# Optimization experiments

Hardware: AMD Instinct MI355X
Metric: run time of the kernel (lower is better)

Reference implementation:

```python
import jax, jax.numpy as jnp
import numpy as np

B, N, D_IMG = 64, 196, 2048
T = 32
V, E, H, A = 32000, 512, 1024, 256
PAD_ID = 0


def setup_inputs() -> dict:
    key = jax.random.key(0)
    ks = jax.random.split(key, 16)
    s = lambda *sh: 1.0 / np.sqrt(sh[-1])
    img_seq = jax.random.normal(ks[0], (B, N, D_IMG), dtype=jnp.float32)
    tokens_in = jax.random.randint(ks[1], (B, T), 0, V, dtype=jnp.int64)
    embed = jax.random.normal(ks[2], (V, E), dtype=jnp.float32) * 0.02
    embed = embed.at[PAD_ID].set(0.0)  # padding_idx row is zero
    W_head1 = jax.random.normal(ks[3], (E, E + D_IMG), dtype=jnp.float32) * s(E + D_IMG)
    W_ih = jax.random.normal(ks[4], (4 * H, E), dtype=jnp.float32) * s(H)
    W_hh = jax.random.normal(ks[5], (4 * H, H), dtype=jnp.float32) * s(H)
    b_ih = jax.random.normal(ks[6], (4 * H,), dtype=jnp.float32) * s(H)
    b_hh = jax.random.normal(ks[7], (4 * H,), dtype=jnp.float32) * s(H)
    W_head = jax.random.normal(ks[8], (V, H), dtype=jnp.float32) * s(H)
    W_img = jax.random.normal(ks[9], (A, D_IMG), dtype=jnp.float32) * s(D_IMG)
    W_hid = jax.random.normal(ks[10], (A, H), dtype=jnp.float32) * s(H)
    w_score = jax.random.normal(ks[11], (A,), dtype=jnp.float32) * s(A)
    W_h0 = jax.random.normal(ks[12], (H, D_IMG), dtype=jnp.float32) * s(D_IMG)
    b_h0 = jax.random.normal(ks[13], (H,), dtype=jnp.float32) * s(D_IMG)
    W_c0 = jax.random.normal(ks[14], (H, D_IMG), dtype=jnp.float32) * s(D_IMG)
    b_c0 = jax.random.normal(ks[15], (H,), dtype=jnp.float32) * s(D_IMG)
    return dict(img_seq=img_seq, tokens_in=tokens_in, embed=embed, W_head1=W_head1,
                W_ih=W_ih, W_hh=W_hh, b_ih=b_ih, b_hh=b_hh, W_head=W_head,
                W_img=W_img, W_hid=W_hid, w_score=w_score,
                W_h0=W_h0, b_h0=b_h0, W_c0=W_c0, b_c0=b_c0)


def _decode(img_seq, tokens_in, embed, W_head1, W_ih, W_hh, b_ih, b_hh,
            W_head, W_img, W_hid, w_score, W_h0, b_h0, W_c0, b_c0):
    g = img_seq.mean(axis=1)                              # [B, D]
    h = jnp.tanh(g @ W_h0.T + b_h0)                       # [B, H]
    c = jnp.tanh(g @ W_c0.T + b_c0)                       # [B, H]
    # image projection is time-invariant: hoist out of the loop
    proj_img = jnp.einsum('bnd,ad->bna', img_seq, W_img)  # [B, N, A]
    emb_all = embed[tokens_in]                            # [B, T, E]

    def step(carry, emb_t):
        h, c = carry
        # additive attention
        proj_h = h @ W_hid.T                              # [B, A]
        scores = jnp.einsum('bna,a->bn', jnp.tanh(proj_img + proj_h[:, None, :]), w_score)
        weights = jax.nn.softmax(scores, axis=-1)         # [B, N]
        ctx = jnp.einsum('bn,bnd->bd', weights, img_seq)  # [B, D]
        x = jnp.concatenate([emb_t, ctx], axis=-1) @ W_head1.T  # [B, E]
        # LSTMCell (PyTorch gate order: i, f, g, o)
        gates = x @ W_ih.T + b_ih + h @ W_hh.T + b_hh     # [B, 4H]
        i, f, gg, o = jnp.split(gates, 4, axis=-1)
        c_new = jax.nn.sigmoid(f) * c + jax.nn.sigmoid(i) * jnp.tanh(gg)
        h_new = jax.nn.sigmoid(o) * jnp.tanh(c_new)
        logits = h_new @ W_head.T                         # [B, V]
        return (h_new, c_new), logits

    _, ys = jax.lax.scan(step, (h, c), jnp.swapaxes(emb_all, 0, 1))  # ys: [T, B, V]
    return jnp.swapaxes(ys, 0, 1)                         # [B, T, V]


def reference(img_seq, tokens_in, embed, W_head1, W_ih, W_hh, b_ih, b_hh,
              W_head, W_img, W_hid, w_score, W_h0, b_h0, W_c0, b_c0):
    return _decode(img_seq, tokens_in, embed, W_head1, W_ih, W_hh, b_ih, b_hh,
                   W_head, W_img, W_hid, w_score, W_h0, b_h0, W_c0, b_c0)
```

## Files before the change

### kernel.cpp

```cpp
#include <hip/hip_runtime.h>
#include <stdint.h>

typedef unsigned short u16;
typedef __bf16 bf16x8 __attribute__((ext_vector_type(8)));
typedef float f32x4 __attribute__((ext_vector_type(4)));

#define DEV static __device__ __forceinline__

DEV u16 f2bu(float f) {
    union { float f; unsigned u; } v; v.f = f;
    unsigned r = v.u + 0x7FFFu + ((v.u >> 16) & 1u);
    return (u16)(r >> 16);
}
DEV float b2f(u16 b) {
    union { unsigned u; float f; } v; v.u = ((unsigned)b) << 16;
    return v.f;
}
DEV float fast_tanh(float x) {
    float e = __expf(2.f * x);
    return 1.f - __fdividef(2.f, e + 1.f);
}
DEV float fast_sig(float x) {
    return __fdividef(1.f, 1.f + __expf(-x));
}
DEV void gload_lds(const u16* g, u16* l) {
    __builtin_amdgcn_global_load_lds((const __attribute__((address_space(1))) void*)g,
                                     (__attribute__((address_space(3))) void*)l, 16, 0, 0);
}

template<bool A_F32, bool B_F32, bool B_KXN, bool OUT_BF16, bool BIAS>
__global__ __launch_bounds__(256) void gemm128(
    const void* __restrict__ Ap, int lda,
    const void* __restrict__ Bp, int ldb,
    void* __restrict__ Cp, int ldc,
    const float* __restrict__ bias, int K)
{
    __shared__ u16 As[128 * 40];
    __shared__ u16 Bs[128 * 40];
    const int tid = threadIdx.x;
    const int lane = tid & 63, wave = tid >> 6;
    const int wr = wave >> 1, wc = wave & 1;
    const int m0 = blockIdx.y * 128, n0 = blockIdx.x * 128;

    f32x4 acc[4][4];
#pragma unroll
    for (int m = 0; m < 4; ++m)
#pragma unroll
        for (int n = 0; n < 4; ++n)
            acc[m][n] = (f32x4){0.f, 0.f, 0.f, 0.f};

    for (int k0 = 0; k0 < K; k0 += 32) {
        __syncthreads();
        if (A_F32) {
            const float* A = (const float*)Ap;
#pragma unroll
            for (int i = 0; i < 4; ++i) {
                int c = tid + i * 256;
                int row = c >> 3, kc = (c & 7) * 4;
                float4 v = *(const float4*)&A[(size_t)(m0 + row) * lda + k0 + kc];
                ushort4 o; o.x = f2bu(v.x); o.y = f2bu(v.y); o.z = f2bu(v.z); o.w = f2bu(v.w);
                *(ushort4*)&As[row * 40 + kc] = o;
            }
        } else {
            const u16* A = (const u16*)Ap;
#pragma unroll
            for (int i = 0; i < 2; ++i) {
                int c = tid + i * 256;
                int row = c >> 2, kc = (c & 3) * 8;
                *(int4*)&As[row * 40 + kc] = *(const int4*)&A[(size_t)(m0 + row) * lda + k0 + kc];
            }
        }
        if (B_KXN) {
            const float* B = (const float*)Bp;
#pragma unroll
            for (int i = 0; i < 4; ++i) {
                int c = tid + i * 256;
                int kk = c >> 5, nc = (c & 31) * 4;
                float4 v = *(const float4*)&B[(size_t)(k0 + kk) * ldb + n0 + nc];
                Bs[(nc + 0) * 40 + kk] = f2bu(v.x);
                Bs[(nc + 1) * 40 + kk] = f2bu(v.y);
                Bs[(nc + 2) * 40 + kk] = f2bu(v.z);
                Bs[(nc + 3) * 40 + kk] = f2bu(v.w);
            }
        } else if (B_F32) {
            const float* B = (const float*)Bp;
#pragma unroll
            for (int i = 0; i < 4; ++i) {
                int c = tid + i * 256;
                int row = c >> 3, kc = (c & 7) * 4;
                float4 v = *(const float4*)&B[(size_t)(n0 + row) * ldb + k0 + kc];
                ushort4 o; o.x = f2bu(v.x); o.y = f2bu(v.y); o.z = f2bu(v.z); o.w = f2bu(v.w);
                *(ushort4*)&Bs[row * 40 + kc] = o;
            }
        } else {
            const u16* B = (const u16*)Bp;
#pragma unroll
            for (int i = 0; i < 2; ++i) {
                int c = tid + i * 256;
                int row = c >> 2, kc = (c & 3) * 8;
                *(int4*)&Bs[row * 40 + kc] = *(const int4*)&B[(size_t)(n0 + row) * ldb + k0 + kc];
            }
        }
        __syncthreads();
        const int fr = lane & 15, kq = (lane >> 4) * 8;
        bf16x8 af[4], bq[4];
#pragma unroll
        for (int m = 0; m < 4; ++m)
            af[m] = *(const bf16x8*)&As[(wr * 64 + m * 16 + fr) * 40 + kq];
#pragma unroll
        for (int n = 0; n < 4; ++n)
            bq[n] = *(const bf16x8*)&Bs[(wc * 64 + n * 16 + fr) * 40 + kq];
#pragma unroll
        for (int m = 0; m < 4; ++m)
#pragma unroll
            for (int n = 0; n < 4; ++n)
                acc[m][n] = __builtin_amdgcn_mfma_f32_16x16x32_bf16(af[m], bq[n], acc[m][n], 0, 0, 0);
    }
    const int fr = lane & 15, rq = (lane >> 4) * 4;
#pragma unroll
    for (int m = 0; m < 4; ++m) {
#pragma unroll
        for (int n = 0; n < 4; ++n) {
            int col = n0 + wc * 64 + n * 16 + fr;
            float bv = BIAS ? bias[col] : 0.f;
#pragma unroll
            for (int r = 0; r < 4; ++r) {
                int row = m0 + wr * 64 + m * 16 + rq + r;
                float v = acc[m][n][r] + bv;
                if (OUT_BF16) ((u16*)Cp)[(size_t)row * ldc + col] = f2bu(v);
                else          ((float*)Cp)[(size_t)row * ldc + col] = v;
            }
        }
    }
}

__global__ __launch_bounds__(512, 4) void gemm_head(const u16* __restrict__ A,
                                                    const u16* __restrict__ B,
                                                    float* __restrict__ C)
{
    __shared__ u16 As[128 * 64];
    __shared__ u16 Bs[256 * 64];
    const int tid = threadIdx.x, lane = tid & 63, wave = tid >> 6;
    const int wr = wave >> 2, wc = wave & 3;
    int bid = blockIdx.x;
    int nb = (bid & 7) * 250 + (bid >> 3);
    const int m0 = (nb & 15) * 128;
    const int n0 = (nb >> 4) * 256;

    f32x4 acc[4][4];
#pragma unroll
    for (int m = 0; m < 4; ++m)
#pragma unroll
        for (int n = 0; n < 4; ++n)
            acc[m][n] = (f32x4){0.f, 0.f, 0.f, 0.f};

    const int srg = lane >> 3;
    const int sslot = lane & 7;
    const int ge = (sslot ^ srg) * 8;
    const int fr = lane & 15, kg = lane >> 4;

    for (int k0 = 0; k0 < 1024; k0 += 64) {
        __syncthreads();
#pragma unroll
        for (int j = 0; j < 2; ++j) {
            const int g = wave * 2 + j;
            gload_lds(&A[(size_t)(m0 + g * 8 + srg) * 1024 + k0 + ge], &As[g * 8 * 64]);
        }
#pragma unroll
        for (int j = 0; j < 4; ++j) {
            const int g = wave * 4 + j;
            gload_lds(&B[(size_t)(n0 + g * 8 + srg) * 1024 + k0 + ge], &Bs[g * 8 * 64]);
        }
        __syncthreads();
#pragma unroll
        for (int kk = 0; kk < 2; ++kk) {
            const int sl = kk * 4 + kg;
            bf16x8 af[4], bq[4];
#pragma unroll
            for (int m = 0; m < 4; ++m) {
                const int row = wr * 64 + m * 16 + fr;
                af[m] = *(const bf16x8*)&As[row * 64 + ((sl ^ (row & 7)) << 3)];
            }
#pragma unroll
            for (int n = 0; n < 4; ++n) {
                const int row = wc * 64 + n * 16 + fr;
                bq[n] = *(const bf16x8*)&Bs[row * 64 + ((sl ^ (row & 7)) << 3)];
            }
#pragma unroll
            for (int m = 0; m < 4; ++m)
#pragma unroll
                for (int n = 0; n < 4; ++n)
                    acc[m][n] = __builtin_amdgcn_mfma_f32_16x16x32_bf16(af[m], bq[n], acc[m][n], 0, 0, 0);
        }
    }
    const int rq = kg * 4;
#pragma unroll
    for (int m = 0; m < 4; ++m)
#pragma unroll
        for (int n = 0; n < 4; ++n) {
            int col = n0 + wc * 64 + n * 16 + fr;
#pragma unroll
            for (int r = 0; r < 4; ++r)
                C[(size_t)(m0 + wr * 64 + m * 16 + rq + r) * 32000 + col] = acc[m][n][r];
        }
}

__global__ __launch_bounds__(256) void prep_k(
    const float* __restrict__ img, const float* __restrict__ Whh,
    const float* __restrict__ Whid, const float* __restrict__ Whead,
    const int* __restrict__ tok, const float* __restrict__ embed,
    const float* __restrict__ bih, const float* __restrict__ bhh,
    u16* __restrict__ img_bf, u16* __restrict__ Whh_bf,
    u16* __restrict__ WhidT, u16* __restrict__ Whead_bf,
    u16* __restrict__ emb_bf, float* __restrict__ bsum)
{
    const int bid = blockIdx.x;
    if (bid < 25088) {
        int i = bid * 256 + threadIdx.x;
        float4 v = ((const float4*)img)[i];
        ushort4 o; o.x = f2bu(v.x); o.y = f2bu(v.y); o.z = f2bu(v.z); o.w = f2bu(v.w);
        ((ushort4*)img_bf)[i] = o;
    } else if (bid < 29184) {
        int i = (bid - 25088) * 256 + threadIdx.x;
        float4 v = ((const float4*)Whh)[i];
        ushort4 o; o.x = f2bu(v.x); o.y = f2bu(v.y); o.z = f2bu(v.z); o.w = f2bu(v.w);
        ((ushort4*)Whh_bf)[i] = o;
    } else if (bid < 29440) {
        int i = (bid - 29184) * 256 + threadIdx.x;
        int a = i >> 8, k4 = (i & 255) * 4;
        float4 v = *(const float4*)&Whid[(size_t)a * 1024 + k4];
        ushort4 o; o.x = f2bu(v.x); o.y = f2bu(v.y); o.z = f2bu(v.z); o.w = f2bu(v.w);
        *(ushort4*)&WhidT[(size_t)(k4 >> 3) * 2048 + a * 8 + (k4 & 7)] = o;
    } else if (bid < 61440) {
        int i = (bid - 29440) * 256 + threadIdx.x;
        float4 v = ((const float4*)Whead)[i];
        ushort4 o; o.x = f2bu(v.x); o.y = f2bu(v.y); o.z = f2bu(v.z); o.w = f2bu(v.w);
        ((ushort4*)Whead_bf)[i] = o;
    } else if (bid < 65536) {
        int id = (bid - 61440) * 256 + threadIdx.x;
        int row = id >> 9, e = id & 511;
        int t = row >> 6, b = row & 63;
        int tk = tok[b * 32 + t];
        emb_bf[(size_t)row * 512 + e] = f2bu(embed[(size_t)tk * 512 + e]);
    } else {
        int i = (bid - 65536) * 256 + threadIdx.x;
        bsum[i] = bih[i] + bhh[i];
    }
}

__global__ __launch_bounds__(256) void pack_w(const u16* __restrict__ Wic,
                                              const u16* __restrict__ Whh,
                                              u16* __restrict__ Wpk)
{
    const int bid = blockIdx.y;
    const int t2 = blockIdx.x * 256 + threadIdx.x;
    const int i = t2 >> 6, lane = t2 & 63;
    const int fr = lane & 15, kq = (lane >> 4) * 8;
    const int grow = ((fr >> 2) << 10) + bid * 4 + (fr & 3);
    const int k0 = i * 32;
    int4 v;
    if (k0 < 2048) v = *(const int4*)&Wic[(size_t)grow * 2048 + k0 + kq];
    else           v = *(const int4*)&Whh[(size_t)grow * 1024 + (k0 - 2048) + kq];
    *(int4*)&Wpk[((size_t)bid * 6144 + t2) * 8] = v;
}

__global__ __launch_bounds__(256) void mean_k(const u16* __restrict__ img_bf, float* __restrict__ gT)
{
    int id = blockIdx.x * 256 + threadIdx.x;
    int b = id >> 10;
    int d = (id & 1023) * 2;
    const u16* base = img_bf + (size_t)b * 196 * 2048 + d;
    float s0 = 0.f, s1 = 0.f;
#pragma unroll 4
    for (int n = 0; n < 196; ++n) {
        ushort2 v = *(const ushort2*)(base + (size_t)n * 2048);
        s0 += b2f(v.x);
        s1 += b2f(v.y);
    }
    gT[(d + 0) * 64 + b] = s0 * (1.f / 196.f);
    gT[(d + 1) * 64 + b] = s1 * (1.f / 196.f);
}

__global__ __launch_bounds__(256) void h0c0(const float* __restrict__ gT,
                                            const float* __restrict__ Wh0, const float* __restrict__ bh0,
                                            const float* __restrict__ Wc0, const float* __restrict__ bc0,
                                            float* __restrict__ c, u16* __restrict__ h0)
{
    int id = blockIdx.x * 256 + threadIdx.x;
    int b = id & 63, n = id >> 6;
    const float4* Wh = (const float4*)&Wh0[(size_t)n * 2048];
    const float4* Wc = (const float4*)&Wc0[(size_t)n * 2048];
    float s0 = 0.f, s1 = 0.f;
#pragma unroll 4
    for (int k4 = 0; k4 < 512; ++k4) {
        float4 wh = Wh[k4], wc = Wc[k4];
        float g0 = gT[(k4 * 4 + 0) * 64 + b];
        float g1 = gT[(k4 * 4 + 1) * 64 + b];
        float g2 = gT[(k4 * 4 + 2) * 64 + b];
        float g3 = gT[(k4 * 4 + 3) * 64 + b];
        s0 += wh.x * g0 + wh.y * g1 + wh.z * g2 + wh.w * g3;
        s1 += wc.x * g0 + wc.y * g1 + wc.z * g2 + wc.w * g3;
    }
    c[b * 1024 + n] = fast_tanh(s1 + bc0[n]);
    h0[(size_t)b * 1024 + n] = f2bu(fast_tanh(s0 + bh0[n]));
}

__global__ __launch_bounds__(1024) void attn_k(const u16* __restrict__ hb,
                                               const u16* __restrict__ WhidT,
                                               const float* __restrict__ w_score,
                                               const u16* __restrict__ proj_bf,
                                               const u16* __restrict__ img_bf,
                                               u16* __restrict__ ctx_bf)
{
    const int b = blockIdx.x >> 2, q = blockIdx.x & 3;
    const int tid = threadIdx.x, lane = tid & 63, wave = tid >> 6;
    __shared__ float ph[256], ws[256], sc[256], red[256];
    __shared__ float hsh[1024];
    __shared__ float php[4][256];
    __shared__ float part[16][512];

    if (tid < 256) {
        ws[tid] = w_score[tid];
        sc[tid] = -1e30f;
    }
    hsh[tid] = b2f(hb[(size_t)b * 1024 + tid]);
    __syncthreads();

    {
        const int a = tid & 255, ks = tid >> 8;
        float s = 0.f;
        const u16* wp = WhidT + a * 8;
#pragma unroll 8
        for (int j = 0; j < 32; ++j) {
            const int kb = ks * 32 + j;
            bf16x8 wv = *(const bf16x8*)(wp + (size_t)kb * 2048);
            const float* hk = &hsh[kb * 8];
#pragma unroll
            for (int i = 0; i < 8; ++i) s += hk[i] * (float)wv[i];
        }
        php[ks][a] = s;
    }
    __syncthreads();
    if (tid < 256) ph[tid] = php[0][tid] + php[1][tid] + php[2][tid] + php[3][tid];
    __syncthreads();

    for (int n = wave; n < 196; n += 16) {
        const int a0 = lane * 4;
        ushort4 pv = *(const ushort4*)&proj_bf[((size_t)b * 196 + n) * 256 + a0];
        float s = ws[a0 + 0] * fast_tanh(b2f(pv.x) + ph[a0 + 0])
                + ws[a0 + 1] * fast_tanh(b2f(pv.y) + ph[a0 + 1])
                + ws[a0 + 2] * fast_tanh(b2f(pv.z) + ph[a0 + 2])
                + ws[a0 + 3] * fast_tanh(b2f(pv.w) + ph[a0 + 3]);
#pragma unroll
        for (int off = 32; off; off >>= 1) s += __shfl_xor(s, off, 64);
        if (lane == 0) sc[n] = s;
    }
    __syncthreads();
    if (tid < 256) red[tid] = sc[tid];
    __syncthreads();
#pragma unroll
    for (int s2 = 128; s2 > 0; s2 >>= 1) {
        if (tid < s2) red[tid] = fmaxf(red[tid], red[tid + s2]);
        __syncthreads();
    }
    const float mx = red[0];
    __syncthreads();
    float e = (tid < 196) ? __expf(sc[tid] - mx) : 0.f;
    if (tid < 256) red[tid] = e;
    __syncthreads();
#pragma unroll
    for (int s2 = 128; s2 > 0; s2 >>= 1) {
        if (tid < s2) red[tid] += red[tid + s2];
        __syncthreads();
    }
    const float inv = __fdividef(1.f, red[0]);
    __syncthreads();
    if (tid < 256) sc[tid] = e * inv;
    __syncthreads();
    const int gid = tid >> 4, st = tid & 15;
    const int c0 = q * 512 + gid * 8;
    const u16* base = img_bf + ((size_t)b * 196) * 2048 + c0;
    float a[8];
#pragma unroll
    for (int i = 0; i < 8; ++i) a[i] = 0.f;
    for (int n = st; n < 196; n += 16) {
        bf16x8 v = *(const bf16x8*)(base + (size_t)n * 2048);
        float wgt = sc[n];
#pragma unroll
        for (int i = 0; i < 8; ++i) a[i] += wgt * (float)v[i];
    }
#pragma unroll
    for (int i = 0; i < 8; ++i) part[st][gid * 8 + i] = a[i];
    __syncthreads();
    if (tid < 512) {
        const int col = tid;
        float v = 0.f;
#pragma unroll
        for (int s16 = 0; s16 < 16; ++s16) v += part[s16][col];
        ctx_bf[(size_t)b * 2048 + q * 512 + col] = f2bu(v);
    }
}

__global__ __launch_bounds__(1024) void gates_k(const u16* __restrict__ ctx_bf,
                                                const u16* __restrict__ hb,
                                                const u16* __restrict__ Wpk,
                                                const float* __restrict__ xg,
                                                float* __restrict__ cbuf,
                                                u16* __restrict__ h_nxt,
                                                u16* __restrict__ h_all,
                                                int t)
{
    const int tid = threadIdx.x, lane = tid & 63, wave = tid >> 6;
    const int fr = lane & 15, kq = (lane >> 4) * 8, rq = (lane >> 4) * 4;
    const int hc0 = blockIdx.x * 4;
    const u16* Wblk = Wpk + (size_t)blockIdx.x * 49152 + lane * 8;
    __shared__ float red[16][64][16];

    f32x4 acc[4];
#pragma unroll
    for (int m = 0; m < 4; ++m) acc[m] = (f32x4){0.f, 0.f, 0.f, 0.f};

    const int kbeg = wave * 192, kend = kbeg + 192;
    const int cend = kend < 2048 ? kend : 2048;
#pragma unroll 2
    for (int k0 = kbeg; k0 < cend; k0 += 32) {
        bf16x8 bq = *(const bf16x8*)&Wblk[(size_t)(k0 >> 5) * 512];
#pragma unroll
        for (int m = 0; m < 4; ++m) {
            bf16x8 af = *(const bf16x8*)&ctx_bf[(size_t)(m * 16 + fr) * 2048 + k0 + kq];
            acc[m] = __builtin_amdgcn_mfma_f32_16x16x32_bf16(af, bq, acc[m], 0, 0, 0);
        }
    }
    const int hbeg = kbeg > 2048 ? kbeg - 2048 : 0;
    const int hend = kend > 2048 ? kend - 2048 : 0;
#pragma unroll 2
    for (int kh = hbeg; kh < hend; kh += 32) {
        bf16x8 bq = *(const bf16x8*)&Wblk[(size_t)((kh + 2048) >> 5) * 512];
#pragma unroll
        for (int m = 0; m < 4; ++m) {
            bf16x8 af = *(const bf16x8*)&hb[(size_t)(m * 16 + fr) * 1024 + kh + kq];
            acc[m] = __builtin_amdgcn_mfma_f32_16x16x32_bf16(af, bq, acc[m], 0, 0, 0);
        }
    }
#pragma unroll
    for (int m = 0; m < 4; ++m)
#pragma unroll
        for (int r = 0; r < 4; ++r)
            red[wave][m * 16 + rq + r][fr] = acc[m][r];
    __syncthreads();

    if (tid < 256) {
        const int bb = tid >> 2, j = tid & 3;
        const int col = hc0 + j;
        float G[4];
#pragma unroll
        for (int g = 0; g < 4; ++g) {
            const int f2 = g * 4 + j;
            float s = 0.f;
#pragma unroll
            for (int w16 = 0; w16 < 16; ++w16) s += red[w16][bb][f2];
            G[g] = s + xg[((size_t)t * 64 + bb) * 4096 + g * 1024 + col];
        }
        float ig = fast_sig(G[0]), fg = fast_sig(G[1]);
        float gv = fast_tanh(G[2]), og = fast_sig(G[3]);
        float cp = cbuf[bb * 1024 + col];
        float cn = fg * cp + ig * gv;
        cbuf[bb * 1024 + col] = cn;
        u16 hv = f2bu(og * fast_tanh(cn));
        h_nxt[(size_t)bb * 1024 + col] = hv;
        h_all[((size_t)bb * 32 + t) * 1024 + col] = hv;
    }
}

extern "C" void kernel_launch(void* const* d_in, const int* in_sizes, int n_in,
                              void* d_out, int out_size, void* d_ws, size_t ws_size,
                              hipStream_t stream)
{
    const float* img     = (const float*)d_in[0];
    const int*   tok     = (const int*)d_in[1];
    const float* embed   = (const float*)d_in[2];
    const float* W_head1 = (const float*)d_in[3];
    const float* W_ih    = (const float*)d_in[4];
    const float* W_hh    = (const float*)d_in[5];
    const float* b_ih    = (const float*)d_in[6];
    const float* b_hh    = (const float*)d_in[7];
    const float* W_head  = (const float*)d_in[8];
    const float* W_img   = (const float*)d_in[9];
    const float* W_hid   = (const float*)d_in[10];
    const float* w_score = (const float*)d_in[11];
    const float* W_h0    = (const float*)d_in[12];
    const float* b_h0    = (const float*)d_in[13];
    const float* W_c0    = (const float*)d_in[14];
    const float* b_c0    = (const float*)d_in[15];
    float* out = (float*)d_out;

    char* w = (char*)d_ws;
    size_t off = 0;
    auto alloc = [&](size_t bytes) { char* p = w + off; off += (bytes + 255) & ~(size_t)255; return p; };

    u16*   Wic      = (u16*)alloc(4096ULL * 2048 * 2);
    u16*   Whh_bf   = (u16*)alloc(4096ULL * 1024 * 2);
    u16*   Wpk      = (u16*)alloc(256ULL * 96 * 64 * 8 * 2);
    u16*   WhidT    = (u16*)alloc(256ULL * 1024 * 2);
    u16*   Whead_bf = (u16*)alloc(32000ULL * 1024 * 2);
    u16*   img_bf   = (u16*)alloc(64ULL * 196 * 2048 * 2);
    float* xg       = (float*)alloc(2048ULL * 4096 * 4);
    u16*   proj_bf  = (u16*)alloc(64ULL * 196 * 256 * 2);
    u16*   emb_bf   = (u16*)alloc(2048ULL * 512 * 2);
    u16*   xe       = (u16*)alloc(2048ULL * 512 * 2);
    float* gT       = (float*)alloc(2048ULL * 64 * 4);
    float* cbuf     = (float*)alloc(64ULL * 1024 * 4);
    u16*   hbuf     = (u16*)alloc(2ULL * 64 * 1024 * 2);
    u16*   ctx_bf   = (u16*)alloc(64ULL * 2048 * 2);
    u16*   h_all    = (u16*)alloc(2048ULL * 1024 * 2);
    float* bsum     = (float*)alloc(4096ULL * 4);
    (void)ws_size; (void)in_sizes; (void)n_in; (void)out_size;

    prep_k<<<dim3(65552), dim3(256), 0, stream>>>(img, W_hh, W_hid, W_head, tok, embed,
                                                  b_ih, b_hh, img_bf, Whh_bf, WhidT,
                                                  Whead_bf, emb_bf, bsum);
    mean_k<<<dim3(256), dim3(256), 0, stream>>>(img_bf, gT);
    h0c0<<<dim3(256), dim3(256), 0, stream>>>(gT, W_h0, b_h0, W_c0, b_c0, cbuf, hbuf);

    gemm128<false, true, false, true, false><<<dim3(4, 16), dim3(256), 0, stream>>>(
        emb_bf, 512, W_head1, 2560, xe, 512, nullptr, 512);
    gemm128<false, true, false, false, true><<<dim3(32, 16), dim3(256), 0, stream>>>(
        xe, 512, W_ih, 512, xg, 4096, bsum, 512);
    gemm128<true, true, true, true, false><<<dim3(16, 32), dim3(256), 0, stream>>>(
        W_ih, 512, W_head1 + 512, 2560, Wic, 2048, nullptr, 512);
    gemm128<false, true, false, true, false><<<dim3(2, 98), dim3(256), 0, stream>>>(
        img_bf, 2048, W_img, 2048, proj_bf, 256, nullptr, 2048);
    pack_w<<<dim3(24, 256), dim3(256), 0, stream>>>(Wic, Whh_bf, Wpk);

    for (int t = 0; t < 32; ++t) {
        u16* hb = hbuf + (size_t)(t & 1) * 65536;
        u16* hn = hbuf + (size_t)((t + 1) & 1) * 65536;
        attn_k<<<dim3(256), dim3(1024), 0, stream>>>(hb, WhidT, w_score, proj_bf, img_bf, ctx_bf);
        gates_k<<<dim3(256), dim3(1024), 0, stream>>>(ctx_bf, hb, Wpk, xg, cbuf, hn, h_all, t);
    }

    gemm_head<<<dim3(2000), dim3(512), 0, stream>>>(h_all, Whead_bf, out);
}
```

Before: 1.941 ms.

## Double-buffer LDS in head GEMM and enlarge tile to 256x256

New measurement: 1.952 ms. About the same (+0.5%).

```diff
diff --git a/kernel.cpp b/kernel.cpp
--- a/kernel.cpp
+++ b/kernel.cpp
@@ -134,18 +134,18 @@
     }
 }
 
-__global__ __launch_bounds__(512, 4) void gemm_head(const u16* __restrict__ A,
-                                                    const u16* __restrict__ B,
-                                                    float* __restrict__ C)
-{
-    __shared__ u16 As[128 * 64];
-    __shared__ u16 Bs[256 * 64];
+__global__ __launch_bounds__(1024) void gemm_head(const u16* __restrict__ A,
+                                                  const u16* __restrict__ B,
+                                                  float* __restrict__ C)
+{
+    __shared__ u16 As[2][256 * 64];
+    __shared__ u16 Bs[2][256 * 64];
     const int tid = threadIdx.x, lane = tid & 63, wave = tid >> 6;
     const int wr = wave >> 2, wc = wave & 3;
     int bid = blockIdx.x;
-    int nb = (bid & 7) * 250 + (bid >> 3);
-    const int m0 = (nb & 15) * 128;
-    const int n0 = (nb >> 4) * 256;
+    int nb = (bid & 7) * 125 + (bid >> 3);
+    const int m0 = (nb & 7) * 256;
+    const int n0 = (nb >> 3) * 256;
 
     f32x4 acc[4][4];
 #pragma unroll
@@ -159,19 +159,24 @@
     const int ge = (sslot ^ srg) * 8;
     const int fr = lane & 15, kg = lane >> 4;
 
-    for (int k0 = 0; k0 < 1024; k0 += 64) {
-        __syncthreads();
-#pragma unroll
-        for (int j = 0; j < 2; ++j) {
-            const int g = wave * 2 + j;
-            gload_lds(&A[(size_t)(m0 + g * 8 + srg) * 1024 + k0 + ge], &As[g * 8 * 64]);
-        }
-#pragma unroll
-        for (int j = 0; j < 4; ++j) {
-            const int g = wave * 4 + j;
-            gload_lds(&B[(size_t)(n0 + g * 8 + srg) * 1024 + k0 + ge], &Bs[g * 8 * 64]);
-        }
-        __syncthreads();
+#define STAGE(bf, kt)                                                              \
+    {                                                                              \
+        const int k0s = (kt) * 64;                                                 \
+        _Pragma("unroll")                                                          \
+        for (int j = 0; j < 2; ++j) {                                              \
+            const int g = wave * 2 + j;                                            \
+            gload_lds(&A[(size_t)(m0 + g * 8 + srg) * 1024 + k0s + ge],            \
+                      &As[bf][g * 8 * 64]);                                        \
+            gload_lds(&B[(size_t)(n0 + g * 8 + srg) * 1024 + k0s + ge],            \
+                      &Bs[bf][g * 8 * 64]);                                        \
+        }                                                                          \
+    }
+
+    STAGE(0, 0);
+    __syncthreads();
+    int cur = 0;
+    for (int kt = 0; kt < 16; ++kt) {
+        if (kt + 1 < 16) STAGE(cur ^ 1, kt + 1);
 #pragma unroll
         for (int kk = 0; kk < 2; ++kk) {
             const int sl = kk * 4 + kg;
@@ -179,12 +184,12 @@
 #pragma unroll
             for (int m = 0; m < 4; ++m) {
                 const int row = wr * 64 + m * 16 + fr;
-                af[m] = *(const bf16x8*)&As[row * 64 + ((sl ^ (row & 7)) << 3)];
+                af[m] = *(const bf16x8*)&As[cur][row * 64 + ((sl ^ (row & 7)) << 3)];
             }
 #pragma unroll
             for (int n = 0; n < 4; ++n) {
                 const int row = wc * 64 + n * 16 + fr;
-                bq[n] = *(const bf16x8*)&Bs[row * 64 + ((sl ^ (row & 7)) << 3)];
+                bq[n] = *(const bf16x8*)&Bs[cur][row * 64 + ((sl ^ (row & 7)) << 3)];
             }
 #pragma unroll
             for (int m = 0; m < 4; ++m)
@@ -192,7 +197,10 @@
                 for (int n = 0; n < 4; ++n)
                     acc[m][n] = __builtin_amdgcn_mfma_f32_16x16x32_bf16(af[m], bq[n], acc[m][n], 0, 0, 0);
         }
-    }
+        __syncthreads();
+        cur ^= 1;
+    }
+#undef STAGE
     const int rq = kg * 4;
 #pragma unroll
     for (int m = 0; m < 4; ++m)
@@ -539,5 +547,5 @@
         gates_k<<<dim3(256), dim3(1024), 0, stream>>>(ctx_bf, hb, Wpk, xg, cbuf, hn, h_all, t);
     }
 
-    gemm_head<<<dim3(2000), dim3(512), 0, stream>>>(h_all, Whead_bf, out);
-}
+    gemm_head<<<dim3(1000), dim3(1024), 0, stream>>>(h_all, Whead_bf, out);
+}
```
